# Optimization experiments

Hardware: AMD Instinct MI355X
Metric: run time of the kernel (lower is better)

## Reference

```python
import jax, jax.numpy as jnp
import numpy as np

D_EMB = 1024
N_HEAD = 16
D_K = D_EMB // N_HEAD


def setup_inputs() -> dict:
    key = jax.random.key(0)
    ks = jax.random.split(key, 11)
    B, S = 2, 2048
    s = 1.0 / np.sqrt(D_EMB)
    inp = {
        'Q': jax.random.normal(ks[0], (B, S, D_EMB), jnp.float32),
        'K': jax.random.normal(ks[1], (B, S, D_EMB), jnp.float32),
        'V': jax.random.normal(ks[2], (B, S, D_EMB), jnp.float32),
        'W_Q': jax.random.normal(ks[3], (D_EMB, D_EMB), jnp.float32) * s,
        'b_Q': jax.random.normal(ks[4], (D_EMB,), jnp.float32) * s,
        'W_K': jax.random.normal(ks[5], (D_EMB, D_EMB), jnp.float32) * s,
        'b_K': jax.random.normal(ks[6], (D_EMB,), jnp.float32) * s,
        'W_V': jax.random.normal(ks[7], (D_EMB, D_EMB), jnp.float32) * s,
        'b_V': jax.random.normal(ks[8], (D_EMB,), jnp.float32) * s,
        'W_O': jax.random.normal(ks[9], (D_EMB, D_EMB), jnp.float32) * s,
        'b_O': jax.random.normal(ks[10], (D_EMB,), jnp.float32) * s,
    }
    return inp


def _heads(x):
    # [B, S, D] -> [B, H, S, d_k]
    B, S, _ = x.shape
    return x.reshape(B, S, N_HEAD, D_K).transpose(0, 2, 1, 3)


def reference(Q, K, V, W_Q, b_Q, W_K, b_K, W_V, b_V, W_O, b_O):
    q = _heads(Q @ W_Q.T + b_Q)
    k = _heads(K @ W_K.T + b_K)
    v = _heads(V @ W_V.T + b_V)
    scale = 1.0 / jnp.sqrt(jnp.asarray(D_K, q.dtype))
    scores = jnp.einsum('bhqd,bhkd->bhqk', q, k) * scale  # [B,H,S,S]
    probs = jax.nn.softmax(scores, axis=-1)
    attn = jnp.einsum('bhqk,bhkd->bhqd', probs, v)
    B, H, S, d = attn.shape
    attn = attn.transpose(0, 2, 1, 3).reshape(B, S, H * d)
    return attn @ W_O.T + b_O
```

## Files before the change

### kernel.cpp

```cpp
#include <hip/hip_runtime.h>
#include <cstdint>
#include <cstddef>

#define S_LEN 2048
#define NH    16
#define DKH   64
#define DEMB  1024
#define MTOT  4096

typedef float f32x4 __attribute__((ext_vector_type(4)));
typedef __bf16 bf16x8 __attribute__((ext_vector_type(8)));
typedef _Float16 f16;
typedef f16 f16x2 __attribute__((ext_vector_type(2)));
typedef f16 f16x4 __attribute__((ext_vector_type(4)));
typedef unsigned short u16;
typedef unsigned int u32;
typedef u16 u16x8 __attribute__((ext_vector_type(8)));
typedef u16 u16x4 __attribute__((ext_vector_type(4)));

static __device__ __forceinline__ u16 f2bf(float f) {
  u32 u = __builtin_bit_cast(u32, f);
  u += 0x7fffu + ((u >> 16) & 1u);
  return (u16)(u >> 16);
}
static __device__ __forceinline__ float bf2f(u16 b) {
  return __builtin_bit_cast(float, ((u32)b) << 16);
}
static __device__ __forceinline__ bf16x8 ldfrag(const u16* p) {
  return __builtin_bit_cast(bf16x8, *(const u16x8*)p);
}
static __device__ __forceinline__ f16x4 ldfragh(const u16* p) {
  return __builtin_bit_cast(f16x4, *(const u16x4*)p);
}
static __device__ __forceinline__ f32x4 mfma16(bf16x8 a, bf16x8 b, f32x4 c) {
  return __builtin_amdgcn_mfma_f32_16x16x32_bf16(a, b, c, 0, 0, 0);
}
static __device__ __forceinline__ f32x4 mfmah(f16x4 a, f16x4 b, f32x4 c) {
  return __builtin_amdgcn_mfma_f32_16x16x16f16(a, b, c, 0, 0, 0);
}
static __device__ __forceinline__ void gl2lds16(const void* g, void* l) {
  __builtin_amdgcn_global_load_lds((__attribute__((address_space(1))) void*)g,
                                   (__attribute__((address_space(3))) void*)l,
                                   16, 0, 0);
}
static __device__ __forceinline__ f16x4 pkh4(float a, float b, float c, float d) {
  f16x2 lo = __builtin_bit_cast(f16x2, __builtin_amdgcn_cvt_pkrtz(a, b));
  f16x2 hi = __builtin_bit_cast(f16x2, __builtin_amdgcn_cvt_pkrtz(c, d));
  return __builtin_shufflevector(lo, hi, 0, 1, 2, 3);
}

#define SCL_Q (0.125f * 1.44269504088896340736f)

__global__ __launch_bounds__(256) void cvt_all(
    const float* __restrict__ wq, const float* __restrict__ wk,
    const float* __restrict__ wv, const float* __restrict__ wo,
    const float* __restrict__ q, const float* __restrict__ k,
    const float* __restrict__ v, u16* __restrict__ dW, u16* __restrict__ dA) {
  int b = blockIdx.x;
  const float* s; u16* d;
  if (b < 4096) {
    const int seg = b >> 10;
    s = (seg == 0) ? wq : (seg == 1) ? wk : (seg == 2) ? wv : wo;
    d = dW + (size_t)seg * (DEMB * DEMB);
    b &= 1023;
  } else {
    const int bb = b - 4096;
    const int seg = bb >> 12;
    s = (seg == 0) ? q : (seg == 1) ? k : v;
    d = dA + (size_t)seg * ((size_t)MTOT * DEMB);
    b = bb & 4095;
  }
  const int i = (b * 256 + threadIdx.x) * 4;
  f32x4 f = *(const f32x4*)(s + i);
  u16x4 o;
  o[0] = f2bf(f[0]); o[1] = f2bf(f[1]); o[2] = f2bf(f[2]); o[3] = f2bf(f[3]);
  *(u16x4*)(d + i) = o;
}

__global__ __launch_bounds__(256) void qkv_gemm(
    const u16* __restrict__ qin, const u16* __restrict__ kin,
    const u16* __restrict__ vin, const u16* __restrict__ W,
    const float* __restrict__ bq, const float* __restrict__ bk,
    const float* __restrict__ bv,
    u16* __restrict__ qh, u16* __restrict__ kh, u16* __restrict__ vt) {
  __shared__ __align__(16) u16 sA[128 * 64];
  __shared__ __align__(16) u16 sB[128 * 64];
  const int t = threadIdx.x;
  const int l = t & 63, w = t >> 6;
  const int ll = l & 15, lg = l >> 4;
  const int nb = blockIdx.x;
  const int mb = blockIdx.y;
  const int which = nb >> 3;
  const u16* A = (which == 0) ? qin : ((which == 1) ? kin : vin);
  const int wr = (w >> 1) * 64, wc = (w & 1) * 64;

  f32x4 acc[4][4] = {};

  for (int kt = 0; kt < 16; ++kt) {
    const int k0 = kt * 64;
    __syncthreads();
#pragma unroll
    for (int i = 0; i < 4; ++i) {
      const int c = i * 256 + t;
      const int row = c >> 3;
      const int gc = (c & 7) ^ (row & 7);
      gl2lds16(A + (size_t)(mb * 128 + row) * DEMB + k0 + gc * 8, &sA[c * 8]);
      gl2lds16(W + (size_t)(nb * 128 + row) * DEMB + k0 + gc * 8, &sB[c * 8]);
    }
    __syncthreads();

#pragma unroll
    for (int kk = 0; kk < 2; ++kk) {
      bf16x8 af[4], bfr[4];
#pragma unroll
      for (int i2 = 0; i2 < 4; ++i2) {
        const int row = wr + i2 * 16 + ll;
        af[i2] = ldfrag(&sA[row * 64 + ((kk * 4 + lg) ^ (row & 7)) * 8]);
      }
#pragma unroll
      for (int j2 = 0; j2 < 4; ++j2) {
        const int row = wc + j2 * 16 + ll;
        bfr[j2] = ldfrag(&sB[row * 64 + ((kk * 4 + lg) ^ (row & 7)) * 8]);
      }
#pragma unroll
      for (int i2 = 0; i2 < 4; ++i2)
#pragma unroll
        for (int j2 = 0; j2 < 4; ++j2)
          acc[i2][j2] = mfma16(af[i2], bfr[j2], acc[i2][j2]);
    }
  }

  const float* bias = (which == 0) ? bq : ((which == 1) ? bk : bv);
  const int b = (mb * 128) >> 11;

  if (which == 2) {
#pragma unroll
    for (int j2 = 0; j2 < 4; ++j2) {
      const int nl = (nb * 128 + wc + j2 * 16 + ll) & 1023;
      const int h = nl >> 6, dk = nl & 63;
      const float bb = bias[nl];
      u16* base = vt + ((size_t)((b * NH + h) * DKH + dk)) * S_LEN;
#pragma unroll
      for (int i2 = 0; i2 < 4; ++i2) {
        const int s = (mb * 128 + wr + i2 * 16 + lg * 4) & 2047;
        const f16x4 pk = pkh4(acc[i2][j2][0] + bb, acc[i2][j2][1] + bb,
                              acc[i2][j2][2] + bb, acc[i2][j2][3] + bb);
        *(u16x4*)&base[s] = __builtin_bit_cast(u16x4, pk);
      }
    }
  } else {
    u16* outp = (which == 0) ? qh : kh;
    const float scl = (which == 0) ? SCL_Q : 1.0f;
#pragma unroll
    for (int j2 = 0; j2 < 4; ++j2) {
      const int nl = (nb * 128 + wc + j2 * 16 + ll) & 1023;
      const int h = nl >> 6, dk = nl & 63;
      const float bb = bias[nl];
#pragma unroll
      for (int i2 = 0; i2 < 4; ++i2) {
#pragma unroll
        for (int r = 0; r < 4; ++r) {
          const int s = (mb * 128 + wr + i2 * 16 + lg * 4 + r) & 2047;
          const float val = (acc[i2][j2][r] + bb) * scl;
          outp[((size_t)((b * NH + h) * S_LEN + s)) * DKH + dk] = f2bf(val);
        }
      }
    }
  }
}

__global__ __launch_bounds__(512, 4) void attn_kernel(
    const u16* __restrict__ qh, const u16* __restrict__ kh,
    const u16* __restrict__ vt, u16* __restrict__ opart,
    float* __restrict__ lpart) {
  __shared__ __align__(16) u16 sK0[64 * 64], sK1[64 * 64];
  __shared__ __align__(16) u16 sV0[64 * 64], sV1[64 * 64];
  const int t = threadIdx.x;
  const int l = t & 63, w = t >> 6;
  const int ll = l & 15, lg = l >> 4;
  const int qb = blockIdx.x >> 1;
  const int ks = blockIdx.x & 1;
  const int q_blk = qb * 256;
  const int bh = blockIdx.y;

  bf16x8 aq[2][2];
#pragma unroll
  for (int qt = 0; qt < 2; ++qt) {
    const u16* qbase =
        qh + ((size_t)bh * S_LEN + q_blk + w * 32 + qt * 16 + ll) * DKH;
    aq[qt][0] = ldfrag(qbase + lg * 8);
    aq[qt][1] = ldfrag(qbase + 32 + lg * 8);
  }

  f32x4 oT[2][4] = {};
  float l_part[2] = {0.f, 0.f};

  const int strow = t >> 3;
  const int sgc = (t & 7) ^ (strow & 7);
  const u16* kstg = kh + ((size_t)bh * S_LEN + ks * 1024 + strow) * DKH + sgc * 8;
  const u16* vstg = vt + ((size_t)bh * DKH + strow) * S_LEN + ks * 1024 + sgc * 8;

  auto stg = [&](int kt, u16* dK, u16* dV) {
    gl2lds16(kstg + (size_t)kt * 64 * DKH, dK + t * 8);
    gl2lds16(vstg + kt * 64, dV + t * 8);
  };

  auto compute = [&](const u16* cK, const u16* cV) {
#pragma unroll
    for (int kbl = 0; kbl < 4; ++kbl) {
      const int krow = kbl * 16 + ll;
      const bf16x8 ak0 = ldfrag(&cK[krow * 64 + (lg ^ (ll & 7)) * 8]);
      const bf16x8 ak1 = ldfrag(&cK[krow * 64 + ((4 + lg) ^ (ll & 7)) * 8]);
      f32x4 s0 = {}, s1 = {};
      s0 = mfma16(ak0, aq[0][0], s0);
      s0 = mfma16(ak1, aq[0][1], s0);
      s1 = mfma16(ak0, aq[1][0], s1);
      s1 = mfma16(ak1, aq[1][1], s1);

      f16x4 bp0, bp1;
      {
        const float p0 = __builtin_amdgcn_exp2f(s0[0]);
        const float p1 = __builtin_amdgcn_exp2f(s0[1]);
        const float p2 = __builtin_amdgcn_exp2f(s0[2]);
        const float p3 = __builtin_amdgcn_exp2f(s0[3]);
        l_part[0] += (p0 + p1) + (p2 + p3);
        bp0 = pkh4(p0, p1, p2, p3);
      }
      {
        const float p0 = __builtin_amdgcn_exp2f(s1[0]);
        const float p1 = __builtin_amdgcn_exp2f(s1[1]);
        const float p2 = __builtin_amdgcn_exp2f(s1[2]);
        const float p3 = __builtin_amdgcn_exp2f(s1[3]);
        l_part[1] += (p0 + p1) + (p2 + p3);
        bp1 = pkh4(p0, p1, p2, p3);
      }

#pragma unroll
      for (int nt = 0; nt < 4; ++nt) {
        const int row = nt * 16 + ll;
        const int ch = (kbl * 2 + (lg >> 1)) ^ (ll & 7);
        const f16x4 av = ldfragh(&cV[row * 64 + ch * 8 + (lg & 1) * 4]);
        oT[0][nt] = mfmah(av, bp0, oT[0][nt]);
        oT[1][nt] = mfmah(av, bp1, oT[1][nt]);
      }
    }
  };

  stg(0, sK0, sV0);
  __syncthreads();
  for (int kt2 = 0; kt2 < 8; ++kt2) {
    stg(2 * kt2 + 1, sK1, sV1);
    compute(sK0, sV0);
    __syncthreads();
    if (kt2 < 7) stg(2 * kt2 + 2, sK0, sV0);
    compute(sK1, sV1);
    __syncthreads();
  }

#pragma unroll
  for (int qt = 0; qt < 2; ++qt) {
    float lv = l_part[qt];
    lv += __shfl_xor(lv, 16, 64);
    lv += __shfl_xor(lv, 32, 64);
    const int orow = q_blk + w * 32 + qt * 16 + ll;
    u16* obase = opart + (((size_t)(ks * 32 + bh)) * S_LEN + orow) * DKH;
#pragma unroll
    for (int nt = 0; nt < 4; ++nt) {
      u16x4 o;
#pragma unroll
      for (int r = 0; r < 4; ++r) o[r] = f2bf(oT[qt][nt][r]);
      *(u16x4*)&obase[nt * 16 + lg * 4] = o;
    }
    if (lg == 0) lpart[(ks * 32 + bh) * S_LEN + orow] = lv;
  }
}

__global__ __launch_bounds__(256) void merge_ctx(
    const u16* __restrict__ op, const float* __restrict__ lp,
    u16* __restrict__ ctx) {
  const int idx = blockIdx.x * 256 + threadIdx.x;
  const int dk8 = idx & 7;
  const int q = (idx >> 3) & 2047;
  const int bh = idx >> 14;
  const float inv = 1.0f / (lp[bh * S_LEN + q] + lp[(32 + bh) * S_LEN + q]);
  const u16x8 a = *(const u16x8*)&op[((size_t)bh * S_LEN + q) * DKH + dk8 * 8];
  const u16x8 c = *(const u16x8*)&op[((size_t)(32 + bh) * S_LEN + q) * DKH + dk8 * 8];
  u16x8 o;
#pragma unroll
  for (int r = 0; r < 8; ++r) o[r] = f2bf((bf2f(a[r]) + bf2f(c[r])) * inv);
  const int b = bh >> 4, h = bh & 15;
  *(u16x8*)&ctx[((size_t)((b * S_LEN + q) * NH + h)) * DKH + dk8 * 8] = o;
}

__global__ __launch_bounds__(256) void out_gemm(
    const u16* __restrict__ Am, const u16* __restrict__ W,
    const float* __restrict__ bo, float* __restrict__ out) {
  __shared__ __align__(16) u16 sA0[128 * 64], sA1[128 * 64];
  __shared__ __align__(16) u16 sB0[64 * 64], sB1[64 * 64];
  const int t = threadIdx.x;
  const int l = t & 63, w = t >> 6;
  const int ll = l & 15, lg = l >> 4;
  const int nb = blockIdx.x;
  const int mb = blockIdx.y;
  const int wr = (w >> 1) * 64, wc = (w & 1) * 32;

  f32x4 acc[4][2] = {};

  auto stg = [&](int kt, u16* dA, u16* dB) {
    const int k0 = kt * 64;
#pragma unroll
    for (int i = 0; i < 4; ++i) {
      const int c = i * 256 + t;
      const int row = c >> 3;
      const int gc = (c & 7) ^ (row & 7);
      gl2lds16(Am + (size_t)(mb * 128 + row) * DEMB + k0 + gc * 8, dA + c * 8);
      if (i < 2)
        gl2lds16(W + (size_t)(nb * 64 + row) * DEMB + k0 + gc * 8, dB + c * 8);
    }
  };

  auto comp = [&](const u16* cA, const u16* cB) {
#pragma unroll
    for (int kk = 0; kk < 2; ++kk) {
      bf16x8 af[4], bfr[2];
#pragma unroll
      for (int i2 = 0; i2 < 4; ++i2) {
        const int row = wr + i2 * 16 + ll;
        af[i2] = ldfrag(&cA[row * 64 + ((kk * 4 + lg) ^ (row & 7)) * 8]);
      }
#pragma unroll
      for (int j2 = 0; j2 < 2; ++j2) {
        const int row = wc + j2 * 16 + ll;
        bfr[j2] = ldfrag(&cB[row * 64 + ((kk * 4 + lg) ^ (row & 7)) * 8]);
      }
#pragma unroll
      for (int i2 = 0; i2 < 4; ++i2)
#pragma unroll
        for (int j2 = 0; j2 < 2; ++j2)
          acc[i2][j2] = mfma16(af[i2], bfr[j2], acc[i2][j2]);
    }
  };

  stg(0, sA0, sB0);
  __syncthreads();
  for (int kt2 = 0; kt2 < 8; ++kt2) {
    stg(2 * kt2 + 1, sA1, sB1);
    comp(sA0, sB0);
    __syncthreads();
    if (kt2 < 7) stg(2 * kt2 + 2, sA0, sB0);
    comp(sA1, sB1);
    __syncthreads();
  }

#pragma unroll
  for (int j2 = 0; j2 < 2; ++j2) {
    const int ncol = nb * 64 + wc + j2 * 16 + ll;
    const float bb = bo[ncol];
#pragma unroll
    for (int i2 = 0; i2 < 4; ++i2) {
#pragma unroll
      for (int r = 0; r < 4; ++r) {
        const int mrow = mb * 128 + wr + i2 * 16 + lg * 4 + r;
        out[(size_t)mrow * DEMB + ncol] = acc[i2][j2][r] + bb;
      }
    }
  }
}

extern "C" void kernel_launch(void* const* d_in, const int* in_sizes, int n_in,
                              void* d_out, int out_size, void* d_ws,
                              size_t ws_size, hipStream_t stream) {
  (void)in_sizes; (void)n_in; (void)out_size; (void)ws_size;
  const float* Q  = (const float*)d_in[0];
  const float* K  = (const float*)d_in[1];
  const float* V  = (const float*)d_in[2];
  const float* WQ = (const float*)d_in[3];
  const float* bQ = (const float*)d_in[4];
  const float* WK = (const float*)d_in[5];
  const float* bK = (const float*)d_in[6];
  const float* WV = (const float*)d_in[7];
  const float* bV = (const float*)d_in[8];
  const float* WO = (const float*)d_in[9];
  const float* bO = (const float*)d_in[10];
  float* out = (float*)d_out;

  u16* ws   = (u16*)d_ws;
  u16* Wqkv = ws;
  u16* Wo   = Wqkv + 3072 * 1024;
  u16* qin  = Wo + 1024 * 1024;
  u16* kin  = qin + (size_t)MTOT * DEMB;
  u16* vin  = kin + (size_t)MTOT * DEMB;
  u16* qh   = vin + (size_t)MTOT * DEMB;
  u16* kh   = qh + 32 * 2048 * 64;
  u16* vt   = kh + 32 * 2048 * 64;
  u16* ctx  = vt + 32 * 2048 * 64;
  u16* opart   = qin;
  float* lpart = (float*)Wqkv;

  cvt_all<<<16384, 256, 0, stream>>>(WQ, WK, WV, WO, Q, K, V, Wqkv, qin);

  qkv_gemm<<<dim3(24, 32), 256, 0, stream>>>(qin, kin, vin, Wqkv, bQ, bK, bV,
                                             qh, kh, vt);
  attn_kernel<<<dim3(16, 32), 512, 0, stream>>>(qh, kh, vt, opart, lpart);
  merge_ctx<<<2048, 256, 0, stream>>>(opart, lpart, ctx);
  out_gemm<<<dim3(16, 32), 256, 0, stream>>>(ctx, Wo, bO, out);
}
```

Baseline: 233.4 us.

## Split attention key range four ways instead of two and merge four partials

The attention kernel now splits each query block's 2048-key range into four 512-key chunks, doubling the grid to 1024 blocks and raising the launch-bounds occupancy hint. Partial outputs go into three slabs carved from the qin workspace plus a fourth placed in the unused upper half of the output buffer. The merge kernel sums four partials and four row sums. The aim is more parallelism and occupancy on the attention stage, paid for by extra partial-output traffic and the per-block Q load and prologue being repeated twice as often.

```diff
diff --git a/kernel.cpp b/kernel.cpp
--- a/kernel.cpp
+++ b/kernel.cpp
@@ -7,6 +7,7 @@
 #define DKH   64
 #define DEMB  1024
 #define MTOT  4096
+#define SLAB  (32 * S_LEN * DKH)
 
 typedef float f32x4 __attribute__((ext_vector_type(4)));
 typedef __bf16 bf16x8 __attribute__((ext_vector_type(8)));
@@ -169,17 +170,17 @@
   }
 }
 
-__global__ __launch_bounds__(512, 4) void attn_kernel(
+__global__ __launch_bounds__(512, 8) void attn_kernel(
     const u16* __restrict__ qh, const u16* __restrict__ kh,
-    const u16* __restrict__ vt, u16* __restrict__ opart,
+    const u16* __restrict__ vt, u16* __restrict__ opA, u16* __restrict__ opB,
     float* __restrict__ lpart) {
   __shared__ __align__(16) u16 sK0[64 * 64], sK1[64 * 64];
   __shared__ __align__(16) u16 sV0[64 * 64], sV1[64 * 64];
   const int t = threadIdx.x;
   const int l = t & 63, w = t >> 6;
   const int ll = l & 15, lg = l >> 4;
-  const int qb = blockIdx.x >> 1;
-  const int ks = blockIdx.x & 1;
+  const int qb = blockIdx.x >> 2;
+  const int ks = blockIdx.x & 3;
   const int q_blk = qb * 256;
   const int bh = blockIdx.y;
 
@@ -197,8 +198,10 @@
 
   const int strow = t >> 3;
   const int sgc = (t & 7) ^ (strow & 7);
-  const u16* kstg = kh + ((size_t)bh * S_LEN + ks * 1024 + strow) * DKH + sgc * 8;
-  const u16* vstg = vt + ((size_t)bh * DKH + strow) * S_LEN + ks * 1024 + sgc * 8;
+  const u16* kstg =
+      kh + ((size_t)bh * S_LEN + ks * 512 + strow) * DKH + sgc * 8;
+  const u16* vstg =
+      vt + ((size_t)bh * DKH + strow) * S_LEN + ks * 512 + sgc * 8;
 
   auto stg = [&](int kt, u16* dK, u16* dV) {
     gl2lds16(kstg + (size_t)kt * 64 * DKH, dK + t * 8);
@@ -248,22 +251,23 @@
 
   stg(0, sK0, sV0);
   __syncthreads();
-  for (int kt2 = 0; kt2 < 8; ++kt2) {
+  for (int kt2 = 0; kt2 < 4; ++kt2) {
     stg(2 * kt2 + 1, sK1, sV1);
     compute(sK0, sV0);
     __syncthreads();
-    if (kt2 < 7) stg(2 * kt2 + 2, sK0, sV0);
+    if (kt2 < 3) stg(2 * kt2 + 2, sK0, sV0);
     compute(sK1, sV1);
     __syncthreads();
   }
 
+  u16* oslab = (ks < 3) ? (opA + (size_t)ks * SLAB) : opB;
 #pragma unroll
   for (int qt = 0; qt < 2; ++qt) {
     float lv = l_part[qt];
     lv += __shfl_xor(lv, 16, 64);
     lv += __shfl_xor(lv, 32, 64);
     const int orow = q_blk + w * 32 + qt * 16 + ll;
-    u16* obase = opart + (((size_t)(ks * 32 + bh)) * S_LEN + orow) * DKH;
+    u16* obase = oslab + ((size_t)bh * S_LEN + orow) * DKH;
 #pragma unroll
     for (int nt = 0; nt < 4; ++nt) {
       u16x4 o;
@@ -276,18 +280,23 @@
 }
 
 __global__ __launch_bounds__(256) void merge_ctx(
-    const u16* __restrict__ op, const float* __restrict__ lp,
-    u16* __restrict__ ctx) {
+    const u16* __restrict__ opA, const u16* __restrict__ opB,
+    const float* __restrict__ lp, u16* __restrict__ ctx) {
   const int idx = blockIdx.x * 256 + threadIdx.x;
   const int dk8 = idx & 7;
   const int q = (idx >> 3) & 2047;
   const int bh = idx >> 14;
-  const float inv = 1.0f / (lp[bh * S_LEN + q] + lp[(32 + bh) * S_LEN + q]);
-  const u16x8 a = *(const u16x8*)&op[((size_t)bh * S_LEN + q) * DKH + dk8 * 8];
-  const u16x8 c = *(const u16x8*)&op[((size_t)(32 + bh) * S_LEN + q) * DKH + dk8 * 8];
+  const float inv = 1.0f / (lp[bh * S_LEN + q] + lp[(32 + bh) * S_LEN + q] +
+                            lp[(64 + bh) * S_LEN + q] + lp[(96 + bh) * S_LEN + q]);
+  const size_t base = ((size_t)bh * S_LEN + q) * DKH + dk8 * 8;
+  const u16x8 a  = *(const u16x8*)&opA[base];
+  const u16x8 b2 = *(const u16x8*)&opA[base + SLAB];
+  const u16x8 c  = *(const u16x8*)&opA[base + 2 * (size_t)SLAB];
+  const u16x8 d  = *(const u16x8*)&opB[base];
   u16x8 o;
 #pragma unroll
-  for (int r = 0; r < 8; ++r) o[r] = f2bf((bf2f(a[r]) + bf2f(c[r])) * inv);
+  for (int r = 0; r < 8; ++r)
+    o[r] = f2bf(((bf2f(a[r]) + bf2f(b2[r])) + (bf2f(c[r]) + bf2f(d[r]))) * inv);
   const int b = bh >> 4, h = bh & 15;
   *(u16x8*)&ctx[((size_t)((b * S_LEN + q) * NH + h)) * DKH + dk8 * 8] = o;
 }
@@ -394,14 +403,15 @@
   u16* kh   = qh + 32 * 2048 * 64;
   u16* vt   = kh + 32 * 2048 * 64;
   u16* ctx  = vt + 32 * 2048 * 64;
-  u16* opart   = qin;
+  u16* opA  = qin;
+  u16* opB  = (u16*)out + (size_t)SLAB;
   float* lpart = (float*)Wqkv;
 
   cvt_all<<<16384, 256, 0, stream>>>(WQ, WK, WV, WO, Q, K, V, Wqkv, qin);
 
   qkv_gemm<<<dim3(24, 32), 256, 0, stream>>>(qin, kin, vin, Wqkv, bQ, bK, bV,
                                              qh, kh, vt);
-  attn_kernel<<<dim3(16, 32), 512, 0, stream>>>(qh, kh, vt, opart, lpart);
-  merge_ctx<<<2048, 256, 0, stream>>>(opart, lpart, ctx);
+  attn_kernel<<<dim3(32, 32), 512, 0, stream>>>(qh, kh, vt, opA, opB, lpart);
+  merge_ctx<<<2048, 256, 0, stream>>>(opA, opB, lpart, ctx);
   out_gemm<<<dim3(16, 32), 256, 0, stream>>>(ctx, Wo, bO, out);
 }
```

Result: slower. 700.0 us (+199.9%).
